# Performance work log

Measured on AMD Instinct MI355X. Metric: run time of the kernel, lower is better.

Reference implementation:

```python
import jax, jax.numpy as jnp
import numpy as np

EPS = 1e-4   # synsin-style z clamp in world_to_view
BIG = 1e10   # z-buffer init


def _xy_grid(h, w):
    xs = jnp.linspace(-1.0, 1.0, w)
    ys = jnp.linspace(-1.0, 1.0, h)
    gy, gx = jnp.meshgrid(ys, xs, indexing='ij')
    return jnp.stack([gx.ravel(), gy.ravel()], 0)  # [2, h*w], NDC pixel rays


def _view_to_world(depth, K_inv, RTinv, xy):
    # depth [B,1,N]; homogeneous coords rows = (x*d, y*d, d, 1)
    proj = jnp.concatenate([xy[None] * depth, depth, jnp.ones_like(depth)], axis=1)  # [B,4,N]
    cam = jnp.einsum('bij,bjn->bin', K_inv, proj)
    return jnp.einsum('bij,bjn->bin', RTinv, cam)  # [B,4,N]


def _world_to_view(world, K, RT):
    cam2 = jnp.einsum('bij,bjn->bin', RT, world)
    xy_proj = jnp.einsum('bij,bjn->bin', K, cam2)
    z = xy_proj[:, 2:3]
    mask = jnp.abs(z) < EPS
    zs = jnp.where(mask, EPS, z)
    sampler = jnp.concatenate([xy_proj[:, 0:2] / zs, z], axis=1)  # [B,3,N]
    return jnp.where(mask, -10.0, sampler)


def _splat_one(sampler, feats, h, w):
    # sampler [3,N] (x,y in NDC, z depth); feats [C,N]. Nearest-pixel z-buffer splat.
    x, y, z = sampler[0], sampler[1], sampler[2]
    n = x.shape[0]
    px = jnp.round((x + 1.0) * 0.5 * (w - 1)).astype(jnp.int32)
    py = jnp.round((y + 1.0) * 0.5 * (h - 1)).astype(jnp.int32)
    valid = (px >= 0) & (px < w) & (py >= 0) & (py < h) & (z > EPS)
    idx = jnp.where(valid, py * w + px, h * w)  # invalid -> dump bucket h*w
    zv = jnp.where(valid, z, BIG)
    zbuf = jnp.full(h * w + 1, BIG, feats.dtype).at[idx].min(zv)
    pid = jnp.where(valid & (zv <= zbuf[idx]), jnp.arange(n, dtype=jnp.int32), n)
    win = jnp.full(h * w + 1, n, jnp.int32).at[idx].min(pid)[: h * w]  # winning point per pixel
    fpad = jnp.concatenate([feats, jnp.zeros((feats.shape[0], 1), feats.dtype)], axis=1)
    out = fpad[:, win].reshape(feats.shape[0], h, w)
    zb = zbuf[: h * w]
    depth = jnp.where(zb < BIG, zb, 0.0).reshape(1, h, w)
    return out, depth


def _project(depths, colors, feats, K, src_RTs, src_RTinvs, dst_RTs, dst_RTinvs):
    B, V, _, Hc, Wc = depths.shape
    _, _, C, Hf, Wf = feats.shape
    sh, sw = Hf / Hc, Wf / Wc
    scale = jnp.array([sw, sh, 1.0, 1.0], depths.dtype)[None, :, None]
    sK = K * scale
    sKinv = jnp.linalg.inv(sK)

    colors_r = jax.image.resize(colors.reshape(B * V, 3, Hc, Wc), (B * V, 3, Hf, Wf),
                                method='linear', antialias=True)
    depths_r = jax.image.resize(depths.reshape(B * V, 1, Hc, Wc), (B * V, 1, Hf, Wf),
                                method='nearest')
    feats_f = feats.reshape(B, V, C, Hf * Wf)
    colors_f = colors_r.reshape(B, V, 3, Hf * Wf)
    depths_f = depths_r.reshape(B, V, 1, Hf * Wf)

    xy = _xy_grid(Hf, Wf)
    dstRT = dst_RTs[:, 0]  # num_outputs == 1
    splat = jax.vmap(lambda s, f: _splat_one(s, f, Hf, Wf))

    results, warped, pdepths = [], [], []
    for i in range(V):  # small fixed number of source views
        world = _view_to_world(depths_f[:, i], sKinv, src_RTinvs[:, i], xy)
        sampler = _world_to_view(world, sK, dstRT)            # [B,3,N]
        src = jnp.concatenate([feats_f[:, i], colors_f[:, i] * 0.5 + 0.5], axis=1)  # [B,C+3,N]
        res, dep = splat(sampler, src)                        # [B,C+3,Hf,Wf], [B,1,Hf,Wf]
        results.append(res[:, :C])
        warped.append(res[:, C:])
        pdepths.append(dep)

    prj_fs = jnp.stack(results, 0)      # [V,B,C,Hf,Wf]
    warped = jnp.stack(warped, 0)       # [V,B,3,Hf,Wf]
    prj_depths = jnp.stack(pdepths, 0)  # [V,B,1,Hf,Wf]
    # forward() permutes prj_fs / prj_depths to [B,V,...]; warped stays [V,B,...]
    return prj_fs.transpose(1, 0, 2, 3, 4), warped, prj_depths.transpose(1, 0, 2, 3, 4)


def setup_inputs() -> dict:
    key = jax.random.key(0)
    k1, k2, k3 = jax.random.split(key, 3)
    B, V, Hc, Wc = 2, 2, 512, 512
    Hf, Wf, C = 256, 256, 64

    depths = jax.random.uniform(k1, (B, V, 1, Hc, Wc), jnp.float32, 1.0, 5.0)
    colors = jax.random.uniform(k2, (B, V, 3, Hc, Wc), jnp.float32, -1.0, 1.0)
    feats = jax.random.normal(k3, (B, V, C, Hf, Wf), jnp.float32)

    K = np.eye(4, dtype=np.float32)  # NDC intrinsic (fx=fy=1, cx=cy=0)
    th = 0.1
    R = np.array([[np.cos(th), 0, np.sin(th), 0.2],
                  [0, 1, 0, 0.0],
                  [-np.sin(th), 0, np.cos(th), 0.1],
                  [0, 0, 0, 1]], dtype=np.float32)
    src_RT = np.eye(4, dtype=np.float32)

    Kb = jnp.asarray(np.tile(K[None], (B, 1, 1)))
    src_RTs = jnp.asarray(np.tile(src_RT[None, None], (B, V, 1, 1)))
    src_RTinvs = src_RTs  # identity
    dst_RTs = jnp.asarray(np.tile(R[None, None], (B, 1, 1, 1)))
    dst_RTinvs = jnp.asarray(np.tile(np.linalg.inv(R)[None, None], (B, 1, 1, 1)))

    return {"depths": depths, "colors": colors, "feats": feats, "K": Kb,
            "src_RTs": src_RTs, "src_RTinvs": src_RTinvs,
            "dst_RTs": dst_RTs, "dst_RTinvs": dst_RTinvs}


def reference(depths, colors, feats, K, src_RTs, src_RTinvs, dst_RTs, dst_RTinvs):
    return _project(depths, colors, feats, K, src_RTs, src_RTinvs, dst_RTs, dst_RTinvs)
```

## Files before the change

kernel.cpp:

```cpp
#include <hip/hip_runtime.h>
#include <stdint.h>

#pragma clang fp contract(off)

namespace {
constexpr int B_ = 2, V_ = 2, HC = 512, WC = 512, HF = 256, WF = 256, CF = 64;
constexpr int NPIX = HF * WF;
constexpr float EPSF = 1e-4f;
constexpr float BIGF = 1e10f;
constexpr int NPT = B_ * V_ * NPIX;
constexpr int NBLK_PT = NPT / 256;
constexpr int RESIZE_BLKS = (B_ * V_ * 3 * NPIX) / 256;
constexpr int TP_BLKS = B_ * V_ * (NPIX / 16);
constexpr size_t WS_BASE = (size_t)NPT * 8 + (size_t)B_ * V_ * 3 * NPIX * 4 + 256;
constexpr size_t TF_BYTES = (size_t)NPT * CF * 4;
}

__device__ __forceinline__ float dot4f(const float* __restrict__ r,
                                       float v0, float v1, float v2, float v3) {
  float t = r[0] * v0;
  t = t + r[1] * v1;
  t = t + r[2] * v2;
  t = t + r[3] * v3;
  return t;
}

__global__ void prep_k(const float* __restrict__ K,
                       const float* __restrict__ colors,
                       float* __restrict__ colr,
                       float* __restrict__ mats,
                       unsigned long long* __restrict__ zwin) {
  int g = blockIdx.x * blockDim.x + threadIdx.x;

  if (g < NPT) zwin[g] = ~0ULL;

  if (g < B_) {
    int b = g;
    const float rowscale[4] = {0.5f, 0.5f, 1.0f, 1.0f};
    float sK[16];
    for (int i = 0; i < 4; ++i)
      for (int j = 0; j < 4; ++j)
        sK[i*4+j] = K[b*16 + i*4 + j] * rowscale[i];
    double m[16];
    for (int i = 0; i < 16; ++i) m[i] = (double)sK[i];
    double inv[16];
    inv[0]  =  m[5]*m[10]*m[15] - m[5]*m[11]*m[14] - m[9]*m[6]*m[15] + m[9]*m[7]*m[14] + m[13]*m[6]*m[11] - m[13]*m[7]*m[10];
    inv[4]  = -m[4]*m[10]*m[15] + m[4]*m[11]*m[14] + m[8]*m[6]*m[15] - m[8]*m[7]*m[14] - m[12]*m[6]*m[11] + m[12]*m[7]*m[10];
    inv[8]  =  m[4]*m[9]*m[15]  - m[4]*m[11]*m[13] - m[8]*m[5]*m[15] + m[8]*m[7]*m[13] + m[12]*m[5]*m[11] - m[12]*m[7]*m[9];
    inv[12] = -m[4]*m[9]*m[14]  + m[4]*m[10]*m[13] + m[8]*m[5]*m[14] - m[8]*m[6]*m[13] - m[12]*m[5]*m[10] + m[12]*m[6]*m[9];
    inv[1]  = -m[1]*m[10]*m[15] + m[1]*m[11]*m[14] + m[9]*m[2]*m[15] - m[9]*m[3]*m[14] - m[13]*m[2]*m[11] + m[13]*m[3]*m[10];
    inv[5]  =  m[0]*m[10]*m[15] - m[0]*m[11]*m[14] - m[8]*m[2]*m[15] + m[8]*m[3]*m[14] + m[12]*m[2]*m[11] - m[12]*m[3]*m[10];
    inv[9]  = -m[0]*m[9]*m[15]  + m[0]*m[11]*m[13] + m[8]*m[1]*m[15] - m[8]*m[3]*m[13] - m[12]*m[1]*m[11] + m[12]*m[3]*m[9];
    inv[13] =  m[0]*m[9]*m[14]  - m[0]*m[10]*m[13] - m[8]*m[1]*m[14] + m[8]*m[2]*m[13] + m[12]*m[1]*m[10] - m[12]*m[2]*m[9];
    inv[2]  =  m[1]*m[6]*m[15]  - m[1]*m[7]*m[14]  - m[5]*m[2]*m[15] + m[5]*m[3]*m[14] + m[13]*m[2]*m[7]  - m[13]*m[3]*m[6];
    inv[6]  = -m[0]*m[6]*m[15]  + m[0]*m[7]*m[14]  + m[4]*m[2]*m[15] - m[4]*m[3]*m[14] - m[12]*m[2]*m[7]  + m[12]*m[3]*m[6];
    inv[10] =  m[0]*m[5]*m[15]  - m[0]*m[7]*m[13]  - m[4]*m[1]*m[15] + m[4]*m[3]*m[13] + m[12]*m[1]*m[7]  - m[12]*m[3]*m[5];
    inv[14] = -m[0]*m[5]*m[14]  + m[0]*m[6]*m[13]  + m[4]*m[1]*m[14] - m[4]*m[2]*m[13] - m[12]*m[1]*m[6]  + m[12]*m[2]*m[5];
    inv[3]  = -m[1]*m[6]*m[11]  + m[1]*m[7]*m[10]  + m[5]*m[2]*m[11] - m[5]*m[3]*m[10] - m[9]*m[2]*m[7]   + m[9]*m[3]*m[6];
    inv[7]  =  m[0]*m[6]*m[11]  - m[0]*m[7]*m[10]  - m[4]*m[2]*m[11] + m[4]*m[3]*m[10] + m[8]*m[2]*m[7]   - m[8]*m[3]*m[6];
    inv[11] = -m[0]*m[5]*m[11]  + m[0]*m[7]*m[9]   + m[4]*m[1]*m[11] - m[4]*m[3]*m[9]  - m[8]*m[1]*m[7]   + m[8]*m[3]*m[5];
    inv[15] =  m[0]*m[5]*m[10]  - m[0]*m[6]*m[9]   - m[4]*m[1]*m[10] + m[4]*m[2]*m[9]  + m[8]*m[1]*m[6]   - m[8]*m[2]*m[5];
    double det = m[0]*inv[0] + m[1]*inv[4] + m[2]*inv[8] + m[3]*inv[12];
    double idet = 1.0 / det;
    for (int i = 0; i < 16; ++i) {
      mats[b*32 + i]      = sK[i];
      mats[b*32 + 16 + i] = (float)(inv[i] * idet);
    }
  }

  if (g >= B_ * V_ * 3 * NPIX) return;
  int pc  = g >> 16;
  int pix = g & (NPIX - 1);
  int y = pix >> 8, x = pix & (WF - 1);
  const float* src = colors + (size_t)pc * HC * WC;
  const float W37 = (float)(3.0 / 7.0), W17 = (float)(1.0 / 7.0);
  float wy[4] = {0.125f, 0.375f, 0.375f, 0.125f};
  float wx[4] = {0.125f, 0.375f, 0.375f, 0.125f};
  if (y == 0)      { wy[0] = 0.f; wy[1] = W37; wy[2] = W37; wy[3] = W17; }
  if (y == HF - 1) { wy[0] = W17; wy[1] = W37; wy[2] = W37; wy[3] = 0.f; }
  if (x == 0)      { wx[0] = 0.f; wx[1] = W37; wx[2] = W37; wx[3] = W17; }
  if (x == WF - 1) { wx[0] = W17; wx[1] = W37; wx[2] = W37; wx[3] = 0.f; }
  int jy0 = 2 * y - 1, jx0 = 2 * x - 1;
  float acc = 0.f;
  #pragma unroll
  for (int ty = 0; ty < 4; ++ty) {
    if (wy[ty] == 0.f) continue;
    int jy = jy0 + ty;
    float rs = 0.f;
    #pragma unroll
    for (int tx = 0; tx < 4; ++tx) {
      if (wx[tx] == 0.f) continue;
      rs = rs + wx[tx] * src[(size_t)jy * WC + (jx0 + tx)];
    }
    acc = acc + wy[ty] * rs;
  }
  colr[g] = acc;
}

__global__ void ts_k(const float* __restrict__ depths,
                     const float* __restrict__ mats,
                     const float* __restrict__ srcRTinv,
                     const float* __restrict__ dstRT,
                     unsigned long long* __restrict__ zwin,
                     const float* __restrict__ feats,
                     float* __restrict__ tf) {
  int bid = blockIdx.x;
  int nT = (int)gridDim.x - NBLK_PT;
  int t = threadIdx.x;

  if (bid < nT) {
    int bv = bid >> 12;
    int pix0 = (bid & 4095) << 4;
    int c4 = t >> 4;
    int p  = t & 15;
    const float* fb = feats + (size_t)bv * CF * NPIX + pix0 + p;
    float4 w;
    w.x = fb[(size_t)(4 * c4 + 0) * NPIX];
    w.y = fb[(size_t)(4 * c4 + 1) * NPIX];
    w.z = fb[(size_t)(4 * c4 + 2) * NPIX];
    w.w = fb[(size_t)(4 * c4 + 3) * NPIX];
    *(float4*)(tf + ((size_t)bv * NPIX + pix0 + p) * CF + 4 * c4) = w;
    return;
  }

  int g = (bid - nT) * 256 + t;
  if (g >= NPT) return;
  int bv = g >> 16;
  int n  = g & (NPIX - 1);
  int b  = bv / V_;
  int y = n >> 8, x = n & (WF - 1);
  float d = depths[(size_t)bv * HC * WC + (size_t)(2 * y + 1) * WC + (2 * x + 1)];
  const float step32 = 2.0f / 255.0f;
  float xf = (float)x * step32 - 1.0f;
  float yf = (float)y * step32 - 1.0f;
  float pr0 = xf * d, pr1 = yf * d, pr2 = d, pr3 = 1.0f;
  const float* sK  = mats + b * 32;
  const float* sKi = mats + b * 32 + 16;
  const float* Rs  = srcRTinv + (size_t)bv * 16;
  const float* Rd  = dstRT + (size_t)b * 16;
  float a0 = dot4f(sKi + 0,  pr0, pr1, pr2, pr3);
  float a1 = dot4f(sKi + 4,  pr0, pr1, pr2, pr3);
  float a2 = dot4f(sKi + 8,  pr0, pr1, pr2, pr3);
  float a3 = dot4f(sKi + 12, pr0, pr1, pr2, pr3);
  float w0 = dot4f(Rs + 0,  a0, a1, a2, a3);
  float w1 = dot4f(Rs + 4,  a0, a1, a2, a3);
  float w2 = dot4f(Rs + 8,  a0, a1, a2, a3);
  float w3 = dot4f(Rs + 12, a0, a1, a2, a3);
  float c0 = dot4f(Rd + 0,  w0, w1, w2, w3);
  float c1 = dot4f(Rd + 4,  w0, w1, w2, w3);
  float c2 = dot4f(Rd + 8,  w0, w1, w2, w3);
  float c3 = dot4f(Rd + 12, w0, w1, w2, w3);
  float p0 = dot4f(sK + 0, c0, c1, c2, c3);
  float p1 = dot4f(sK + 4, c0, c1, c2, c3);
  float p2 = dot4f(sK + 8, c0, c1, c2, c3);
  if (!(p2 > EPSF)) return;
  float sx = p0 / p2, sy = p1 / p2;
  float pxf = rintf(((sx + 1.0f) * 0.5f) * 255.0f);
  float pyf = rintf(((sy + 1.0f) * 0.5f) * 255.0f);
  if (!(pxf >= 0.0f && pxf <= 255.0f && pyf >= 0.0f && pyf <= 255.0f)) return;
  int idx = (int)pyf * WF + (int)pxf;
  unsigned zbits = __float_as_uint(p2);
  unsigned long long key = ((unsigned long long)zbits << 32) | (unsigned)n;
  atomicMin(&zwin[(size_t)bv * NPIX + idx], key);
}

__global__ void gatherT_k(const unsigned long long* __restrict__ zwin,
                          const float* __restrict__ tf,
                          const float* __restrict__ colr,
                          float* __restrict__ out0,
                          float* __restrict__ out1,
                          float* __restrict__ out2) {
  int bid = blockIdx.x;
  int grp = bid >> 10;
  int g   = (bid & (NBLK_PT - 1)) * 256 + threadIdx.x;
  int bv  = g >> 16;
  int pix = g & (NPIX - 1);
  unsigned long long key = zwin[g];
  bool hit = (key != ~0ULL);
  int n = (int)(key & 0xffffffffULL);

  if (grp < 4) {
    float4 f[4];
    if (hit) {
      const float4* src =
          (const float4*)(tf + ((size_t)bv * NPIX + n) * CF + grp * 16);
      #pragma unroll
      for (int i = 0; i < 4; ++i) f[i] = src[i];
    } else {
      #pragma unroll
      for (int i = 0; i < 4; ++i) f[i] = make_float4(0.f, 0.f, 0.f, 0.f);
    }
    float* o0 = out0 + (size_t)bv * CF * NPIX + (size_t)(grp * 16) * NPIX + pix;
    const float* fs = (const float*)f;
    #pragma unroll
    for (int c = 0; c < 16; ++c)
      __builtin_nontemporal_store(fs[c], &o0[(size_t)c * NPIX]);
  } else {
    int b = bv >> 1, v = bv & 1;
    const float* cb = colr + (size_t)bv * 3 * NPIX;
    float* o1 = out1 + (size_t)(v * B_ + b) * 3 * NPIX + pix;
    if (hit) {
      float z = __uint_as_float((unsigned)(key >> 32));
      __builtin_nontemporal_store((z < BIGF) ? z : 0.0f, &out2[g]);
      #pragma unroll
      for (int ch = 0; ch < 3; ++ch)
        __builtin_nontemporal_store(cb[(size_t)ch * NPIX + n] * 0.5f + 0.5f,
                                    &o1[(size_t)ch * NPIX]);
    } else {
      __builtin_nontemporal_store(0.0f, &out2[g]);
      #pragma unroll
      for (int ch = 0; ch < 3; ++ch)
        __builtin_nontemporal_store(0.0f, &o1[(size_t)ch * NPIX]);
    }
  }
}

__global__ void gather_k(const unsigned long long* __restrict__ zwin,
                         const float* __restrict__ feats,
                         const float* __restrict__ colr,
                         float* __restrict__ out0,
                         float* __restrict__ out1,
                         float* __restrict__ out2) {
  int bid = blockIdx.x;
  int grp = bid >> 10;
  int g   = (bid & (NBLK_PT - 1)) * 256 + threadIdx.x;
  int bv  = g >> 16;
  int pix = g & (NPIX - 1);
  unsigned long long key = zwin[g];
  bool hit = (key != ~0ULL);
  int n = (int)(key & 0xffffffffULL);

  if (grp < 4) {
    int c0 = grp * 16;
    const float* fb = feats + (size_t)bv * CF * NPIX + (size_t)c0 * NPIX;
    float* o0 = out0 + (size_t)bv * CF * NPIX + (size_t)c0 * NPIX + pix;
    if (hit) {
      #pragma unroll
      for (int c = 0; c < 16; ++c)
        __builtin_nontemporal_store(fb[(size_t)c * NPIX + n], &o0[(size_t)c * NPIX]);
    } else {
      #pragma unroll
      for (int c = 0; c < 16; ++c)
        __builtin_nontemporal_store(0.0f, &o0[(size_t)c * NPIX]);
    }
  } else {
    int b = bv >> 1, v = bv & 1;
    const float* cb = colr + (size_t)bv * 3 * NPIX;
    float* o1 = out1 + (size_t)(v * B_ + b) * 3 * NPIX + pix;
    if (hit) {
      float z = __uint_as_float((unsigned)(key >> 32));
      __builtin_nontemporal_store((z < BIGF) ? z : 0.0f, &out2[g]);
      #pragma unroll
      for (int ch = 0; ch < 3; ++ch)
        __builtin_nontemporal_store(cb[(size_t)ch * NPIX + n] * 0.5f + 0.5f,
                                    &o1[(size_t)ch * NPIX]);
    } else {
      __builtin_nontemporal_store(0.0f, &out2[g]);
      #pragma unroll
      for (int ch = 0; ch < 3; ++ch)
        __builtin_nontemporal_store(0.0f, &o1[(size_t)ch * NPIX]);
    }
  }
}

extern "C" void kernel_launch(void* const* d_in, const int* in_sizes, int n_in,
                              void* d_out, int out_size, void* d_ws, size_t ws_size,
                              hipStream_t stream) {
  const float* depths     = (const float*)d_in[0];
  const float* colors     = (const float*)d_in[1];
  const float* feats      = (const float*)d_in[2];
  const float* K          = (const float*)d_in[3];
  const float* src_RTinvs = (const float*)d_in[5];
  const float* dst_RTs    = (const float*)d_in[6];

  float* out0 = (float*)d_out;
  float* out1 = out0 + (size_t)B_ * V_ * CF * NPIX;
  float* out2 = out1 + (size_t)V_ * B_ * 3 * NPIX;

  unsigned long long* zwin = (unsigned long long*)d_ws;
  float* colr = (float*)(zwin + NPT);
  float* mats = colr + (size_t)B_ * V_ * 3 * NPIX;
  float* tf   = (float*)((char*)d_ws + WS_BASE);

  const bool use_tf = (ws_size >= WS_BASE + TF_BYTES);

  prep_k<<<RESIZE_BLKS, 256, 0, stream>>>(K, colors, colr, mats, zwin);
  int ts_grid = use_tf ? (TP_BLKS + NBLK_PT) : NBLK_PT;
  ts_k<<<ts_grid, 256, 0, stream>>>(depths, mats, src_RTinvs, dst_RTs, zwin, feats, tf);
  if (use_tf)
    gatherT_k<<<5 * NBLK_PT, 256, 0, stream>>>(zwin, tf, colr, out0, out1, out2);
  else
    gather_k<<<5 * NBLK_PT, 256, 0, stream>>>(zwin, feats, colr, out0, out1, out2);
}
```

Measured before the change: 188.9 us.

## Merge color resize into transpose/splat kernel and widen transpose and gather tiles

The color downsample moves out of the init kernel and into the combined work kernel, so the init kernel only clears the z-buffer and builds the matrices, and the resize runs alongside the feature transpose and the splat. The transpose now handles 64 pixels per block with float4 loads and an in-register 4x4 transpose, where it used to handle 16 pixels with scalar loads. The gather kernel now copies 32 channels per thread instead of 16, so it launches 3 block groups instead of 5. These changes aim to cut serialization and improve memory coalescing, at the cost of more registers per gather thread and mixed block types in one launch.

```diff
diff --git a/kernel.cpp b/kernel.cpp
--- a/kernel.cpp
+++ b/kernel.cpp
@@ -11,7 +11,7 @@
 constexpr int NPT = B_ * V_ * NPIX;
 constexpr int NBLK_PT = NPT / 256;
 constexpr int RESIZE_BLKS = (B_ * V_ * 3 * NPIX) / 256;
-constexpr int TP_BLKS = B_ * V_ * (NPIX / 16);
+constexpr int TP_BLKS = B_ * V_ * (NPIX / 64);
 constexpr size_t WS_BASE = (size_t)NPT * 8 + (size_t)B_ * V_ * 3 * NPIX * 4 + 256;
 constexpr size_t TF_BYTES = (size_t)NPT * CF * 4;
 }
@@ -25,14 +25,11 @@
   return t;
 }
 
-__global__ void prep_k(const float* __restrict__ K,
-                       const float* __restrict__ colors,
-                       float* __restrict__ colr,
+__global__ void init_k(const float* __restrict__ K,
                        float* __restrict__ mats,
                        unsigned long long* __restrict__ zwin) {
   int g = blockIdx.x * blockDim.x + threadIdx.x;
-
-  if (g < NPT) zwin[g] = ~0ULL;
+  zwin[g] = ~0ULL;
 
   if (g < B_) {
     int b = g;
@@ -67,63 +64,72 @@
       mats[b*32 + 16 + i] = (float)(inv[i] * idet);
     }
   }
-
-  if (g >= B_ * V_ * 3 * NPIX) return;
-  int pc  = g >> 16;
-  int pix = g & (NPIX - 1);
-  int y = pix >> 8, x = pix & (WF - 1);
-  const float* src = colors + (size_t)pc * HC * WC;
-  const float W37 = (float)(3.0 / 7.0), W17 = (float)(1.0 / 7.0);
-  float wy[4] = {0.125f, 0.375f, 0.375f, 0.125f};
-  float wx[4] = {0.125f, 0.375f, 0.375f, 0.125f};
-  if (y == 0)      { wy[0] = 0.f; wy[1] = W37; wy[2] = W37; wy[3] = W17; }
-  if (y == HF - 1) { wy[0] = W17; wy[1] = W37; wy[2] = W37; wy[3] = 0.f; }
-  if (x == 0)      { wx[0] = 0.f; wx[1] = W37; wx[2] = W37; wx[3] = W17; }
-  if (x == WF - 1) { wx[0] = W17; wx[1] = W37; wx[2] = W37; wx[3] = 0.f; }
-  int jy0 = 2 * y - 1, jx0 = 2 * x - 1;
-  float acc = 0.f;
-  #pragma unroll
-  for (int ty = 0; ty < 4; ++ty) {
-    if (wy[ty] == 0.f) continue;
-    int jy = jy0 + ty;
-    float rs = 0.f;
+}
+
+__global__ void work_k(const float* __restrict__ depths,
+                       const float* __restrict__ mats,
+                       const float* __restrict__ srcRTinv,
+                       const float* __restrict__ dstRT,
+                       unsigned long long* __restrict__ zwin,
+                       const float* __restrict__ feats,
+                       float* __restrict__ tf,
+                       const float* __restrict__ colors,
+                       float* __restrict__ colr) {
+  int bid = blockIdx.x;
+  int nTP = (int)gridDim.x - RESIZE_BLKS - NBLK_PT;
+  int t = threadIdx.x;
+
+  if (bid < nTP) {
+    int bv = bid >> 10;
+    int pix0 = (bid & 1023) << 6;
+    int c4 = t >> 4;
+    int p4 = t & 15;
+    const float* fb = feats + (size_t)bv * CF * NPIX + pix0 + 4 * p4;
+    float4 v0 = *(const float4*)(fb + (size_t)(4 * c4 + 0) * NPIX);
+    float4 v1 = *(const float4*)(fb + (size_t)(4 * c4 + 1) * NPIX);
+    float4 v2 = *(const float4*)(fb + (size_t)(4 * c4 + 2) * NPIX);
+    float4 v3 = *(const float4*)(fb + (size_t)(4 * c4 + 3) * NPIX);
+    float* tb = tf + ((size_t)bv * NPIX + pix0 + 4 * p4) * CF + 4 * c4;
+    *(float4*)(tb + 0 * CF) = make_float4(v0.x, v1.x, v2.x, v3.x);
+    *(float4*)(tb + 1 * CF) = make_float4(v0.y, v1.y, v2.y, v3.y);
+    *(float4*)(tb + 2 * CF) = make_float4(v0.z, v1.z, v2.z, v3.z);
+    *(float4*)(tb + 3 * CF) = make_float4(v0.w, v1.w, v2.w, v3.w);
+    return;
+  }
+
+  int rb = bid - nTP;
+  if (rb < RESIZE_BLKS) {
+    int g = rb * 256 + t;
+    int pc  = g >> 16;
+    int pix = g & (NPIX - 1);
+    int y = pix >> 8, x = pix & (WF - 1);
+    const float* src = colors + (size_t)pc * HC * WC;
+    const float W37 = (float)(3.0 / 7.0), W17 = (float)(1.0 / 7.0);
+    float wy[4] = {0.125f, 0.375f, 0.375f, 0.125f};
+    float wx[4] = {0.125f, 0.375f, 0.375f, 0.125f};
+    if (y == 0)      { wy[0] = 0.f; wy[1] = W37; wy[2] = W37; wy[3] = W17; }
+    if (y == HF - 1) { wy[0] = W17; wy[1] = W37; wy[2] = W37; wy[3] = 0.f; }
+    if (x == 0)      { wx[0] = 0.f; wx[1] = W37; wx[2] = W37; wx[3] = W17; }
+    if (x == WF - 1) { wx[0] = W17; wx[1] = W37; wx[2] = W37; wx[3] = 0.f; }
+    int jy0 = 2 * y - 1, jx0 = 2 * x - 1;
+    float acc = 0.f;
     #pragma unroll
-    for (int tx = 0; tx < 4; ++tx) {
-      if (wx[tx] == 0.f) continue;
-      rs = rs + wx[tx] * src[(size_t)jy * WC + (jx0 + tx)];
-    }
-    acc = acc + wy[ty] * rs;
-  }
-  colr[g] = acc;
-}
-
-__global__ void ts_k(const float* __restrict__ depths,
-                     const float* __restrict__ mats,
-                     const float* __restrict__ srcRTinv,
-                     const float* __restrict__ dstRT,
-                     unsigned long long* __restrict__ zwin,
-                     const float* __restrict__ feats,
-                     float* __restrict__ tf) {
-  int bid = blockIdx.x;
-  int nT = (int)gridDim.x - NBLK_PT;
-  int t = threadIdx.x;
-
-  if (bid < nT) {
-    int bv = bid >> 12;
-    int pix0 = (bid & 4095) << 4;
-    int c4 = t >> 4;
-    int p  = t & 15;
-    const float* fb = feats + (size_t)bv * CF * NPIX + pix0 + p;
-    float4 w;
-    w.x = fb[(size_t)(4 * c4 + 0) * NPIX];
-    w.y = fb[(size_t)(4 * c4 + 1) * NPIX];
-    w.z = fb[(size_t)(4 * c4 + 2) * NPIX];
-    w.w = fb[(size_t)(4 * c4 + 3) * NPIX];
-    *(float4*)(tf + ((size_t)bv * NPIX + pix0 + p) * CF + 4 * c4) = w;
+    for (int ty = 0; ty < 4; ++ty) {
+      if (wy[ty] == 0.f) continue;
+      int jy = jy0 + ty;
+      float rs = 0.f;
+      #pragma unroll
+      for (int tx = 0; tx < 4; ++tx) {
+        if (wx[tx] == 0.f) continue;
+        rs = rs + wx[tx] * src[(size_t)jy * WC + (jx0 + tx)];
+      }
+      acc = acc + wy[ty] * rs;
+    }
+    colr[g] = acc;
     return;
   }
 
-  int g = (bid - nT) * 256 + t;
+  int g = (rb - RESIZE_BLKS) * 256 + t;
   if (g >= NPT) return;
   int bv = g >> 16;
   int n  = g & (NPIX - 1);
@@ -164,7 +170,7 @@
   atomicMin(&zwin[(size_t)bv * NPIX + idx], key);
 }
 
-__global__ void gatherT_k(const unsigned long long* __restrict__ zwin,
+__global__ void gather3_k(const unsigned long long* __restrict__ zwin,
                           const float* __restrict__ tf,
                           const float* __restrict__ colr,
                           float* __restrict__ out0,
@@ -179,21 +185,21 @@
   bool hit = (key != ~0ULL);
   int n = (int)(key & 0xffffffffULL);
 
-  if (grp < 4) {
-    float4 f[4];
+  if (grp < 2) {
+    float4 f[8];
     if (hit) {
       const float4* src =
-          (const float4*)(tf + ((size_t)bv * NPIX + n) * CF + grp * 16);
-      #pragma unroll
-      for (int i = 0; i < 4; ++i) f[i] = src[i];
+          (const float4*)(tf + ((size_t)bv * NPIX + n) * CF + grp * 32);
+      #pragma unroll
+      for (int i = 0; i < 8; ++i) f[i] = src[i];
     } else {
       #pragma unroll
-      for (int i = 0; i < 4; ++i) f[i] = make_float4(0.f, 0.f, 0.f, 0.f);
-    }
-    float* o0 = out0 + (size_t)bv * CF * NPIX + (size_t)(grp * 16) * NPIX + pix;
+      for (int i = 0; i < 8; ++i) f[i] = make_float4(0.f, 0.f, 0.f, 0.f);
+    }
+    float* o0 = out0 + (size_t)bv * CF * NPIX + (size_t)(grp * 32) * NPIX + pix;
     const float* fs = (const float*)f;
     #pragma unroll
-    for (int c = 0; c < 16; ++c)
+    for (int c = 0; c < 32; ++c)
       __builtin_nontemporal_store(fs[c], &o0[(size_t)c * NPIX]);
   } else {
     int b = bv >> 1, v = bv & 1;
@@ -284,11 +290,12 @@
 
   const bool use_tf = (ws_size >= WS_BASE + TF_BYTES);
 
-  prep_k<<<RESIZE_BLKS, 256, 0, stream>>>(K, colors, colr, mats, zwin);
-  int ts_grid = use_tf ? (TP_BLKS + NBLK_PT) : NBLK_PT;
-  ts_k<<<ts_grid, 256, 0, stream>>>(depths, mats, src_RTinvs, dst_RTs, zwin, feats, tf);
+  init_k<<<NBLK_PT, 256, 0, stream>>>(K, mats, zwin);
+  int work_grid = (use_tf ? TP_BLKS : 0) + RESIZE_BLKS + NBLK_PT;
+  work_k<<<work_grid, 256, 0, stream>>>(depths, mats, src_RTinvs, dst_RTs, zwin,
+                                        feats, tf, colors, colr);
   if (use_tf)
-    gatherT_k<<<5 * NBLK_PT, 256, 0, stream>>>(zwin, tf, colr, out0, out1, out2);
+    gather3_k<<<3 * NBLK_PT, 256, 0, stream>>>(zwin, tf, colr, out0, out1, out2);
   else
     gather_k<<<5 * NBLK_PT, 256, 0, stream>>>(zwin, feats, colr, out0, out1, out2);
 }
```

Result: faster. 181.5 us (-3.9%).
